# Kernel optimization log

Hardware: AMD Instinct MI355X
Metric: run time of the kernel (lower is better)

The kernel has to match this reference:

```python
import jax, jax.numpy as jnp
import numpy as np

N_NODES = 50000
N_EDGES = 800000
IN_FEAT = 128
HEADS = 8
HEAD_DIM = 16  # out_feat // num_heads = 128 // 8
NEG_SLOPE = 0.2


def setup_inputs() -> dict:
    key = jax.random.key(0)
    ks = jax.random.split(key, 8)
    g = 1.0 / np.sqrt(IN_FEAT)
    return {
        "x": jax.random.normal(ks[0], (N_NODES, IN_FEAT), jnp.float32),
        "efeat": jax.random.normal(ks[1], (N_EDGES, IN_FEAT), jnp.float32),
        "src": jax.random.randint(ks[2], (N_EDGES,), 0, N_NODES),
        "dst": jax.random.randint(ks[3], (N_EDGES,), 0, N_NODES),
        "W_src": jax.random.normal(ks[4], (HEADS * HEAD_DIM, IN_FEAT), jnp.float32) * g,
        "b_src": jnp.zeros((HEADS * HEAD_DIM,), jnp.float32),
        "W_dst": jax.random.normal(ks[5], (HEADS * HEAD_DIM, IN_FEAT), jnp.float32) * g,
        "b_dst": jnp.zeros((HEADS * HEAD_DIM,), jnp.float32),
        "W_edge": jax.random.normal(ks[6], (HEADS * HEAD_DIM, IN_FEAT), jnp.float32) * g,
        "attn": jax.random.normal(ks[7], (HEADS, HEAD_DIM), jnp.float32) * (1.0 / np.sqrt(HEAD_DIM)),
    }


def reference(x, efeat, src, dst, W_src, b_src, W_dst, b_dst, W_edge, attn):
    H, D = HEADS, HEAD_DIM
    # node/edge projections: [N,H,D] / [E,H,D]
    feat_src = (x @ W_src.T + b_src).reshape(-1, H, D)
    feat_dst = (x @ W_dst.T + b_dst).reshape(-1, H, D)
    feat_edge = (efeat @ W_edge.T).reshape(-1, H, D)

    # per-edge GATv2 score: LeakyReLU(src + dst + edge) . attn  -> [E,H]
    fs = feat_src[src]                                    # gather [E,H,D]
    tmp = fs + feat_dst[dst] + feat_edge
    e = jnp.where(tmp >= 0, tmp, NEG_SLOPE * tmp)
    score = jnp.einsum('ehd,hd->eh', e, attn)

    # edge softmax normalized per destination node
    m = jax.ops.segment_max(score, dst, num_segments=N_NODES)     # [N,H]
    ex = jnp.exp(score - jax.lax.stop_gradient(m)[dst])
    z = jax.ops.segment_sum(ex, dst, num_segments=N_NODES)        # [N,H]
    a = ex / z[dst]                                               # [E,H]

    # weighted scatter-sum of (src + edge) messages
    msg = (fs + feat_edge) * a[:, :, None]                        # [E,H,D]
    h = jax.ops.segment_sum(msg, dst, num_segments=N_NODES)       # [N,H,D]

    # res_fc is None since in_feat == H*D; activation = relu
    h = jax.nn.relu(h)
    return h.reshape(N_NODES, H * D)
```

## Files before the change

kernel.cpp:

```cpp
#include <hip/hip_runtime.h>
#include <hip/hip_bf16.h>

#define NNODES 50000
#define NEDGES 800000
#define NEG_SLOPE 0.2f
#define N_PAD 50176

typedef float f32x4 __attribute__((ext_vector_type(4)));
typedef float f32x2 __attribute__((ext_vector_type(2)));
typedef __bf16 bf16x8 __attribute__((ext_vector_type(8)));
typedef __bf16 bf16x4 __attribute__((ext_vector_type(4)));
typedef __bf16 bf16x2 __attribute__((ext_vector_type(2)));

__global__ __launch_bounds__(256) void convert_hist(
    const float* __restrict__ W0, const float* __restrict__ W1,
    const float* __restrict__ W2, __bf16* __restrict__ out,
    const int* __restrict__ dst, int* __restrict__ deg, int* __restrict__ arr)
{
  int b = blockIdx.x;
  if (b < 48) {
    int m = b >> 4;
    const float* W = (m == 0) ? W0 : ((m == 1) ? W1 : W2);
    __bf16* o = out + m * 16384;
    int i = (b & 15) * 1024 + threadIdx.x * 4;
    int r = i >> 7, cx = i & 127;
    f32x4 v = *(const f32x4*)(W + i);
    int kb = cx >> 3, ko = cx & 7;
    int off = r * 128 + ((kb ^ (r & 15)) << 3) + ko;
    bf16x4 pk = { (__bf16)v.x, (__bf16)v.y, (__bf16)v.z, (__bf16)v.w };
    *(bf16x4*)(o + off) = pk;
  } else {
    int e = (b - 48) * 256 + threadIdx.x;
    arr[e] = atomicAdd(&deg[dst[e]], 1);
  }
}

__global__ void scan_local(const int* __restrict__ deg, int* __restrict__ scanned,
                           int* __restrict__ bsum){
  __shared__ int s[1024];
  int t = threadIdx.x, i = blockIdx.x * 1024 + t;
  int v = deg[i];
  s[t] = v; __syncthreads();
  #pragma unroll
  for (int off = 1; off < 1024; off <<= 1){
    int x = (t >= off) ? s[t - off] : 0;
    __syncthreads();
    s[t] += x;
    __syncthreads();
  }
  scanned[i] = s[t] - v;
  if (t == 1023) bsum[blockIdx.x] = s[t];
}

__device__ __forceinline__ void gemm_core(
    int m0, const float* __restrict__ A, const __bf16* __restrict__ Wsw,
    int M, __bf16* sS, f32x4 (&acc)[2][8])
{
  const int t = threadIdx.x;
  const int w = t >> 6, lane = t & 63;
  const int rsel = lane & 15, quad = lane >> 4;

  bf16x8 wreg[8];
  #pragma unroll
  for (int it = 0; it < 8; ++it)
    wreg[it] = *(const bf16x8*)(Wsw + it * 2048 + t * 8);

  f32x4 r0[2][4], r1[2][4];
  #pragma unroll
  for (int mi = 0; mi < 2; ++mi) {
    int gr = m0 + w * 32 + mi * 16 + rsel;
    const float* p = A + (size_t)gr * 128 + (quad << 3);
    bool ok = gr < M;
    #pragma unroll
    for (int kk = 0; kk < 4; ++kk) {
      f32x4 z4 = {0.f, 0.f, 0.f, 0.f};
      r0[mi][kk] = ok ? *(const f32x4*)(p + kk * 32)     : z4;
      r1[mi][kk] = ok ? *(const f32x4*)(p + kk * 32 + 4) : z4;
    }
  }

  #pragma unroll
  for (int it = 0; it < 8; ++it)
    *(bf16x8*)(sS + it * 2048 + t * 8) = wreg[it];

  bf16x8 af[4][2];
  #pragma unroll
  for (int mi = 0; mi < 2; ++mi)
    #pragma unroll
    for (int kk = 0; kk < 4; ++kk)
      af[kk][mi] = (bf16x8){ (__bf16)r0[mi][kk].x, (__bf16)r0[mi][kk].y,
                             (__bf16)r0[mi][kk].z, (__bf16)r0[mi][kk].w,
                             (__bf16)r1[mi][kk].x, (__bf16)r1[mi][kk].y,
                             (__bf16)r1[mi][kk].z, (__bf16)r1[mi][kk].w };

  f32x4 zero = {0.f, 0.f, 0.f, 0.f};
  #pragma unroll
  for (int mi = 0; mi < 2; ++mi)
    #pragma unroll
    for (int ni = 0; ni < 8; ++ni) acc[mi][ni] = zero;

  __syncthreads();

  #pragma unroll
  for (int kk = 0; kk < 4; ++kk) {
    int kb0 = kk * 4 + quad;
    bf16x8 bfr[8];
    #pragma unroll
    for (int ni = 0; ni < 8; ++ni) {
      int r = ni * 16 + rsel;
      bfr[ni] = *(const bf16x8*)(sS + r * 128 + ((kb0 ^ (r & 15)) << 3));
    }
    #pragma unroll
    for (int mi = 0; mi < 2; ++mi)
      #pragma unroll
      for (int ni = 0; ni < 8; ++ni)
        acc[mi][ni] = __builtin_amdgcn_mfma_f32_16x16x32_bf16(af[kk][mi], bfr[ni], acc[mi][ni], 0, 0, 0);
  }
}

__global__ __launch_bounds__(256, 4) void scan_nodes(
    const int* __restrict__ scanned, const int* __restrict__ bsum,
    int* __restrict__ row_start,
    const float* __restrict__ x, const __bf16* __restrict__ wsw,
    const float* __restrict__ b_src, const float* __restrict__ b_dst,
    float* __restrict__ feat_src, float* __restrict__ feat_dst)
{
  __shared__ __bf16 sS[128 * 136];
  __shared__ int sbase;
  int b = blockIdx.x;
  if (b < 196) {
    int t = threadIdx.x;
    if (t == 0){
      int lim = b >> 2, a = 0;
      for (int j = 0; j < lim; ++j) a += bsum[j];
      sbase = a;
    }
    __syncthreads();
    int i = b * 256 + t;
    if (i < N_PAD) row_start[i] = scanned[i] + sbase;
    return;
  }
  const float* bias; float* outp; int m0; const __bf16* wp;
  if (b < 587) { m0 = (b - 196) * 128; bias = b_src; outp = feat_src; wp = wsw; }
  else         { m0 = (b - 587) * 128; bias = b_dst; outp = feat_dst; wp = wsw + 16384; }

  f32x4 acc[2][8];
  gemm_core(m0, x, wp, NNODES, sS, acc);

  const int t = threadIdx.x;
  const int w = t >> 6, lane = t & 63;
  const int rsel = lane & 15, quad = lane >> 4;
  #pragma unroll
  for (int mi = 0; mi < 2; ++mi)
    #pragma unroll
    for (int ni = 0; ni < 8; ++ni)
      #pragma unroll
      for (int r4 = 0; r4 < 4; ++r4) {
        int grow = m0 + w * 32 + mi * 16 + quad * 4 + r4;
        int col = ni * 16 + rsel;
        if (grow < NNODES)
          outp[(size_t)grow * 128 + col] = acc[mi][ni][r4] + bias[col];
      }
}

__global__ __launch_bounds__(256, 4) void proj_edge(
    const float* __restrict__ efeat, const __bf16* __restrict__ Wsw,
    const int* __restrict__ src, const int* __restrict__ dst,
    const int* __restrict__ arr, const int* __restrict__ row_start,
    const float* __restrict__ fs, __bf16* __restrict__ msg)
{
  __shared__ __bf16 sS[128 * 136];
  const int t = threadIdx.x;
  const int m0 = blockIdx.x * 128;

  int tr = t >> 1, h = t & 1;
  int e = m0 + tr;
  int s = src[e];
  int pos = row_start[dst[e]] + arr[e];

  f32x4 acc[2][8];
  gemm_core(m0, efeat, Wsw, NEDGES, sS, acc);

  const int w = t >> 6, lane = t & 63;
  const int rsel = lane & 15, quad = lane >> 4;

  __syncthreads();
  #pragma unroll
  for (int mi = 0; mi < 2; ++mi)
    #pragma unroll
    for (int ni = 0; ni < 8; ++ni)
      #pragma unroll
      for (int r4 = 0; r4 < 4; ++r4) {
        float v = acc[mi][ni][r4];
        float vx = __shfl_xor(v, 1);
        if (!(rsel & 1)) {
          int trow = w * 32 + mi * 16 + quad * 4 + r4;
          bf16x2 pkv = { (__bf16)v, (__bf16)vx };
          *(bf16x2*)(sS + trow * 136 + ni * 16 + rsel) = pkv;
        }
      }
  __syncthreads();

  const float* fsp = fs + (size_t)s * 128 + h * 64;
  const __bf16* sp = sS + tr * 136 + h * 64;
  __bf16* dp = msg + (size_t)pos * 128 + h * 64;
  #pragma unroll
  for (int half = 0; half < 2; ++half) {
    f32x4 fr[8];
    #pragma unroll
    for (int i = 0; i < 8; ++i)
      fr[i] = *(const f32x4*)(fsp + half * 32 + i * 4);
    #pragma unroll
    for (int i = 0; i < 4; ++i) {
      bf16x8 ev = *(const bf16x8*)(sp + half * 32 + i * 8);
      bf16x8 mv;
      #pragma unroll
      for (int j = 0; j < 8; ++j)
        mv[j] = (__bf16)(fr[i * 2 + (j >> 2)][j & 3] + (float)ev[j]);
      *(bf16x8*)(dp + half * 32 + i * 8) = mv;
    }
  }
}

__global__ __launch_bounds__(256) void aggregate_msg(
    const int* __restrict__ row_start, const int* __restrict__ deg,
    const __bf16* __restrict__ msg, const float* __restrict__ fd,
    const float* __restrict__ attn, float* __restrict__ out)
{
  int wv = threadIdx.x >> 6, lane = threadIdx.x & 63;
  int n = blockIdx.x * 4 + wv;
  int row = row_start[n], dg = deg[n];
  int c = lane << 1;
  f32x2 fdv = *(const f32x2*)(fd + (size_t)n * 128 + c);
  f32x2 atv = *(const f32x2*)(attn + c);
  float a0 = 0.f, a1 = 0.f, zs = 0.f;
  const __bf16* mp = msg + (size_t)row * 128 + c;

  #define EDGE_BODY(MV)                                                \
    {                                                                  \
      float v0 = (float)(MV).x, v1 = (float)(MV).y;                    \
      float t0 = v0 + fdv.x; t0 = t0 >= 0.f ? t0 : NEG_SLOPE * t0;     \
      float t1 = v1 + fdv.y; t1 = t1 >= 0.f ? t1 : NEG_SLOPE * t1;     \
      float p = t0 * atv.x + t1 * atv.y;                               \
      p += __shfl_xor(p, 1);                                           \
      p += __shfl_xor(p, 2);                                           \
      p += __shfl_xor(p, 4);                                           \
      float ex = __expf(p);                                            \
      a0 += ex * v0; a1 += ex * v1; zs += ex;                          \
    }

  int j = 0;
  for (; j + 8 <= dg; j += 8) {
    bf16x2 mv[8];
    #pragma unroll
    for (int u = 0; u < 8; ++u) mv[u] = *(const bf16x2*)(mp + (size_t)(j + u) * 128);
    #pragma unroll
    for (int u = 0; u < 8; ++u) EDGE_BODY(mv[u])
  }
  for (; j < dg; ++j) {
    bf16x2 mv = *(const bf16x2*)(mp + (size_t)j * 128);
    EDGE_BODY(mv)
  }
  #undef EDGE_BODY

  float rz = zs > 0.f ? 1.f / zs : 0.f;
  float o0 = a0 * rz, o1 = a1 * rz;
  f32x2 ov = { o0 > 0.f ? o0 : 0.f, o1 > 0.f ? o1 : 0.f };
  *(f32x2*)(out + (size_t)n * 128 + c) = ov;
}

extern "C" void kernel_launch(void* const* d_in, const int* in_sizes, int n_in,
                              void* d_out, int out_size, void* d_ws, size_t ws_size,
                              hipStream_t stream)
{
  const float* x      = (const float*)d_in[0];
  const float* efeat  = (const float*)d_in[1];
  const int*   src    = (const int*)d_in[2];
  const int*   dst    = (const int*)d_in[3];
  const float* W_src  = (const float*)d_in[4];
  const float* b_src  = (const float*)d_in[5];
  const float* W_dst  = (const float*)d_in[6];
  const float* b_dst  = (const float*)d_in[7];
  const float* W_edge = (const float*)d_in[8];
  const float* attn   = (const float*)d_in[9];

  char* ws = (char*)d_ws;
  float*  feat_src  = (float*)(ws + 0);
  float*  feat_dst  = (float*)(ws + 25600000);
  __bf16* msg       = (__bf16*)(ws + 51200000);
  int*    arr       = (int*)  (ws + 256000000);
  int*    row_start = (int*)  (ws + 259200000);
  int*    scanned   = (int*)  (ws + 259400704);
  int*    deg       = (int*)  (ws + 259601408);
  int*    bsum      = (int*)  (ws + 259802112);
  __bf16* wsw       = (__bf16*)(ws + 259803136);

  hipMemsetAsync(deg, 0, 200704, stream);

  convert_hist<<<3173, 256, 0, stream>>>(W_src, W_dst, W_edge, wsw, dst, deg, arr);

  scan_local<<<49, 1024, 0, stream>>>(deg, scanned, bsum);

  scan_nodes<<<978, 256, 0, stream>>>(scanned, bsum, row_start, x, wsw,
                                      b_src, b_dst, feat_src, feat_dst);

  proj_edge<<<6250, 256, 0, stream>>>(efeat, wsw + 32768, src, dst, arr, row_start,
                                      feat_src, msg);

  aggregate_msg<<<12500, 256, 0, stream>>>(row_start, deg, msg, feat_dst, attn,
                                           (float*)d_out);
}
```

Measured before the change: 782.1 us.

## Build CSR edge-id map and gather edge features in dst order

Adds a scatter kernel that writes, for each CSR position, the original edge id. proj_edge then walks CSR positions: it gathers efeat rows by edge id and writes msg contiguously, where before it read efeat sequentially and scattered msg writes. The efeat fragments are loaded straight into registers instead of going through gemm_core. Blocks are also remapped to tiles per XCD so that neighbouring tiles share an XCD's L2. The cost is an extra kernel launch and reads of efeat rows in random order.

```diff
diff --git a/kernel.cpp b/kernel.cpp
--- a/kernel.cpp
+++ b/kernel.cpp
@@ -163,26 +163,91 @@
       }
 }
 
+__global__ void scatter_eid(const int* __restrict__ dst, const int* __restrict__ arr,
+                            const int* __restrict__ row_start, int* __restrict__ csr_eid){
+  int e = blockIdx.x * 256 + threadIdx.x;
+  csr_eid[row_start[dst[e]] + arr[e]] = e;
+}
+
 __global__ __launch_bounds__(256, 4) void proj_edge(
     const float* __restrict__ efeat, const __bf16* __restrict__ Wsw,
-    const int* __restrict__ src, const int* __restrict__ dst,
-    const int* __restrict__ arr, const int* __restrict__ row_start,
+    const int* __restrict__ src, const int* __restrict__ csr_eid,
     const float* __restrict__ fs, __bf16* __restrict__ msg)
 {
   __shared__ __bf16 sS[128 * 136];
   const int t = threadIdx.x;
-  const int m0 = blockIdx.x * 128;
+  int b = blockIdx.x;
+  int xcd = b & 7, bi = b >> 3;
+  int tile = (xcd < 2 ? xcd * 782 : 1564 + (xcd - 2) * 781) + bi;
+  const int m0 = tile * 128;
 
   int tr = t >> 1, h = t & 1;
-  int e = m0 + tr;
-  int s = src[e];
-  int pos = row_start[dst[e]] + arr[e];
-
-  f32x4 acc[2][8];
-  gemm_core(m0, efeat, Wsw, NEDGES, sS, acc);
+  int ep_e = csr_eid[m0 + tr];
+  int s = src[ep_e];
 
   const int w = t >> 6, lane = t & 63;
   const int rsel = lane & 15, quad = lane >> 4;
+
+  int p0 = m0 + w * 32 + rsel;
+  int e0 = csr_eid[p0];
+  int e1 = csr_eid[p0 + 16];
+
+  bf16x8 wreg[8];
+  #pragma unroll
+  for (int it = 0; it < 8; ++it)
+    wreg[it] = *(const bf16x8*)(Wsw + it * 2048 + t * 8);
+
+  f32x4 r0[2][4], r1[2][4];
+  {
+    const float* pa0 = efeat + (size_t)e0 * 128 + (quad << 3);
+    const float* pa1 = efeat + (size_t)e1 * 128 + (quad << 3);
+    #pragma unroll
+    for (int kk = 0; kk < 4; ++kk) {
+      r0[0][kk] = *(const f32x4*)(pa0 + kk * 32);
+      r1[0][kk] = *(const f32x4*)(pa0 + kk * 32 + 4);
+      r0[1][kk] = *(const f32x4*)(pa1 + kk * 32);
+      r1[1][kk] = *(const f32x4*)(pa1 + kk * 32 + 4);
+    }
+  }
+
+  #pragma unroll
+  for (int it = 0; it < 8; ++it)
+    *(bf16x8*)(sS + it * 2048 + t * 8) = wreg[it];
+
+  bf16x8 af[4][2];
+  #pragma unroll
+  for (int mi = 0; mi < 2; ++mi)
+    #pragma unroll
+    for (int kk = 0; kk < 4; ++kk)
+      af[kk][mi] = (bf16x8){ (__bf16)r0[mi][kk].x, (__bf16)r0[mi][kk].y,
+                             (__bf16)r0[mi][kk].z, (__bf16)r0[mi][kk].w,
+                             (__bf16)r1[mi][kk].x, (__bf16)r1[mi][kk].y,
+                             (__bf16)r1[mi][kk].z, (__bf16)r1[mi][kk].w };
+
+  f32x4 acc[2][8];
+  f32x4 zero = {0.f, 0.f, 0.f, 0.f};
+  #pragma unroll
+  for (int mi = 0; mi < 2; ++mi)
+    #pragma unroll
+    for (int ni = 0; ni < 8; ++ni) acc[mi][ni] = zero;
+
+  __syncthreads();
+
+  #pragma unroll
+  for (int kk = 0; kk < 4; ++kk) {
+    int kb0 = kk * 4 + quad;
+    bf16x8 bfr[8];
+    #pragma unroll
+    for (int ni = 0; ni < 8; ++ni) {
+      int r = ni * 16 + rsel;
+      bfr[ni] = *(const bf16x8*)(sS + r * 128 + ((kb0 ^ (r & 15)) << 3));
+    }
+    #pragma unroll
+    for (int mi = 0; mi < 2; ++mi)
+      #pragma unroll
+      for (int ni = 0; ni < 8; ++ni)
+        acc[mi][ni] = __builtin_amdgcn_mfma_f32_16x16x32_bf16(af[kk][mi], bfr[ni], acc[mi][ni], 0, 0, 0);
+  }
 
   __syncthreads();
   #pragma unroll
@@ -203,7 +268,7 @@
 
   const float* fsp = fs + (size_t)s * 128 + h * 64;
   const __bf16* sp = sS + tr * 136 + h * 64;
-  __bf16* dp = msg + (size_t)pos * 128 + h * 64;
+  __bf16* dp = msg + (size_t)(m0 + tr) * 128 + h * 64;
   #pragma unroll
   for (int half = 0; half < 2; ++half) {
     f32x4 fr[8];
@@ -289,11 +354,12 @@
   float*  feat_dst  = (float*)(ws + 25600000);
   __bf16* msg       = (__bf16*)(ws + 51200000);
   int*    arr       = (int*)  (ws + 256000000);
-  int*    row_start = (int*)  (ws + 259200000);
-  int*    scanned   = (int*)  (ws + 259400704);
-  int*    deg       = (int*)  (ws + 259601408);
-  int*    bsum      = (int*)  (ws + 259802112);
-  __bf16* wsw       = (__bf16*)(ws + 259803136);
+  int*    csr_eid   = (int*)  (ws + 259200000);
+  int*    row_start = (int*)  (ws + 262400000);
+  int*    scanned   = (int*)  (ws + 262600704);
+  int*    deg       = (int*)  (ws + 262801408);
+  int*    bsum      = (int*)  (ws + 263002112);
+  __bf16* wsw       = (__bf16*)(ws + 263003136);
 
   hipMemsetAsync(deg, 0, 200704, stream);
 
@@ -304,7 +370,9 @@
   scan_nodes<<<978, 256, 0, stream>>>(scanned, bsum, row_start, x, wsw,
                                       b_src, b_dst, feat_src, feat_dst);
 
-  proj_edge<<<6250, 256, 0, stream>>>(efeat, wsw + 32768, src, dst, arr, row_start,
+  scatter_eid<<<3125, 256, 0, stream>>>(dst, arr, row_start, csr_eid);
+
+  proj_edge<<<6250, 256, 0, stream>>>(efeat, wsw + 32768, src, csr_eid,
                                       feat_src, msg);
 
   aggregate_msg<<<12500, 256, 0, stream>>>(row_start, deg, msg, feat_dst, attn,
```

After: 782.6 us. About the same (+0.1%).
